# Optimization experiments

Measured on AMD Instinct MI355X. Metric: run time of the kernel, lower is better.

## Reference

```python
import jax, jax.numpy as jnp
import numpy as np
import math

B, S, D, H = 2, 2048, 1024, 16
DH = D // H
FF = 4096
EPS = 1e-5


def _xavier(k, shape):
    lim = math.sqrt(6.0 / (shape[0] + shape[1]))
    return jax.random.uniform(k, shape, jnp.float32, -lim, lim)


def setup_inputs() -> dict:
    key = jax.random.key(0)
    ks = jax.random.split(key, 8)
    return {
        "x": jax.random.normal(ks[0], (B, S, D), jnp.float32),
        "mask": jnp.ones((B, S), jnp.int32),
        "WQ": _xavier(ks[1], (D, D)), "bQ": jnp.zeros((D,), jnp.float32),
        "WK": _xavier(ks[2], (D, D)), "bK": jnp.zeros((D,), jnp.float32),
        "WV": _xavier(ks[3], (D, D)), "bV": jnp.zeros((D,), jnp.float32),
        "WY": _xavier(ks[4], (D, D)), "bY": jnp.zeros((D,), jnp.float32),
        "ln1_w": jnp.ones((D,), jnp.float32), "ln1_b": jnp.zeros((D,), jnp.float32),
        "ln2_w": jnp.ones((D,), jnp.float32), "ln2_b": jnp.zeros((D,), jnp.float32),
        "W1": _xavier(ks[5], (D, FF)), "b1": jnp.zeros((FF,), jnp.float32),
        "W2": _xavier(ks[6], (FF, D)), "b2": jnp.zeros((D,), jnp.float32),
    }


def _layer_norm(x, w, b):
    # manual LayerNorm: biased variance over last dim
    m = jnp.mean(x, axis=-1, keepdims=True)
    v = jnp.mean(jnp.square(x - m), axis=-1, keepdims=True)
    return (x - m) / jnp.sqrt(v + EPS) * w + b


def _attention(x, mask, WQ, bQ, WK, bK, WV, bV, WY, bY):
    b, s, _ = x.shape
    def split(t):  # (B,S,D) -> (B,H,S,DH)
        return t.reshape(b, s, H, DH).transpose(0, 2, 1, 3)
    q = split(x @ WQ + bQ)
    k = split(x @ WK + bK)
    v = split(x @ WV + bV)
    scores = jnp.einsum('bhqd,bhkd->bhqk', q, k) / math.sqrt(DH)
    scores = jnp.where(mask[:, None, None, :] == 0, -jnp.inf, scores)
    w = jax.nn.softmax(scores, axis=-1)
    y = jnp.einsum('bhqk,bhkd->bhqd', w, v)
    y = y.transpose(0, 2, 1, 3).reshape(b, s, D)  # merge heads
    return y @ WY + bY


def reference(x, mask, WQ, bQ, WK, bK, WV, bV, WY, bY,
              ln1_w, ln1_b, ln2_w, ln2_b, W1, b1, W2, b2):
    a = _attention(x, mask, WQ, bQ, WK, bK, WV, bV, WY, bY)
    h = _layer_norm(a + x, ln1_w, ln1_b)
    ff = jax.nn.gelu(h @ W1 + b1, approximate=False) @ W2 + b2
    return _layer_norm(ff + h, ln2_w, ln2_b)
```

## Files before the change

### kernel.cpp

```cpp
#include <hip/hip_runtime.h>
#include <cstdint>
#include <cstddef>

#define B_ 2
#define S_ 2048
#define D_ 1024
#define H_ 16
#define DH_ 64
#define FF_ 4096
#define M_ (B_*S_)
#define MB_ ((size_t)1 << 20)
#define NT_ (S_/64)

using u16 = unsigned short;
using short8 = __attribute__((ext_vector_type(8))) short;
using short4v = __attribute__((ext_vector_type(4))) short;
using floatx4 = __attribute__((ext_vector_type(4))) float;

__device__ __forceinline__ float bf2f(u16 u) {
    return __uint_as_float(((uint32_t)u) << 16);
}
__device__ __forceinline__ u16 f2bf(float f) {
    uint32_t u = __float_as_uint(f);
    u += 0x7fffu + ((u >> 16) & 1u);
    return (u16)(u >> 16);
}
__device__ __forceinline__ uint32_t cvtpk_bf16(float lo, float hi) {
    uint32_t r;
    asm("v_cvt_pk_bf16_f32 %0, %1, %2" : "=v"(r) : "v"(lo), "v"(hi));
    return r;
}
__device__ __forceinline__ void async_copy16(const u16* g, u16* l) {
    __builtin_amdgcn_global_load_lds(
        (const __attribute__((address_space(1))) uint32_t*)g,
        (__attribute__((address_space(3))) uint32_t*)l, 16, 0, 0);
}

__device__ __forceinline__ void gemm_step(
    const u16* Acur, const u16* Bcur, u16* Astg, u16* Bstg, bool pref,
    const u16*& gA, const u16*& gB, int K,
    int w, int wm, int wn, int lm, int quad, floatx4 (&acc)[4][4])
{
    if (pref) {
        async_copy16(gA, Astg + w * 512);
        async_copy16(gA + (size_t)64 * K, Astg + w * 512 + 2048);
        async_copy16(gB, Bstg + w * 512);
        async_copy16(gB + (size_t)64 * K, Bstg + w * 512 + 2048);
        gA += 32; gB += 32;
    }
    short8 af[4], bfr[4];
#pragma unroll
    for (int t4 = 0; t4 < 4; ++t4)
        af[t4] = *(const short8*)&Acur[(wm * 64 + t4 * 16 + lm) * 32 + quad * 8];
#pragma unroll
    for (int t4 = 0; t4 < 4; ++t4)
        bfr[t4] = *(const short8*)&Bcur[(wn * 64 + t4 * 16 + lm) * 32 + quad * 8];
#pragma unroll
    for (int i = 0; i < 4; ++i)
#pragma unroll
        for (int j = 0; j < 4; ++j)
            acc[i][j] = __builtin_amdgcn_mfma_f32_16x16x32_bf16(
                af[i], bfr[j], acc[i][j], 0, 0, 0);
    __syncthreads();
}

__global__ __launch_bounds__(256) void cvt_f32_bf16(
    const float* __restrict__ in, u16* __restrict__ out, int n)
{
    const int i = (blockIdx.x * 256 + threadIdx.x) * 4;
    if (i < n) {
        const float4 v = *(const float4*)(in + i);
        out[i + 0] = f2bf(v.x);
        out[i + 1] = f2bf(v.y);
        out[i + 2] = f2bf(v.z);
        out[i + 3] = f2bf(v.w);
    }
}

__global__ __launch_bounds__(256) void mask_bias(
    const int* __restrict__ mask, float* __restrict__ bias, int n)
{
    const int i = blockIdx.x * 256 + threadIdx.x;
    if (i < n) bias[i] = mask[i] ? 0.f : -1e30f;
}

__global__ void transpose_cvt(const float* __restrict__ in, u16* __restrict__ out,
                              int R, int C) {
    __shared__ float t[32][33];
    const int bx = blockIdx.x * 32, by = blockIdx.y * 32;
    const int tx = threadIdx.x, ty = threadIdx.y;
#pragma unroll
    for (int i = 0; i < 32; i += 8)
        t[ty + i][tx] = in[(size_t)(by + ty + i) * C + bx + tx];
    __syncthreads();
#pragma unroll
    for (int i = 0; i < 32; i += 8)
        out[(size_t)(bx + ty + i) * R + by + tx] = f2bf(t[tx][ty + i]);
}

__global__ void transpose_cvt4(
    const float* __restrict__ WQ, const float* __restrict__ WK,
    const float* __restrict__ WV, const float* __restrict__ WY,
    u16* __restrict__ Wqkvt, u16* __restrict__ WYt)
{
    __shared__ float t[32][33];
    const int zz = blockIdx.z;
    const float* in = zz == 0 ? WQ : zz == 1 ? WK : zz == 2 ? WV : WY;
    u16* out = zz < 3 ? Wqkvt + (size_t)zz * D_ * D_ : WYt;
    const int bx = blockIdx.x * 32, by = blockIdx.y * 32;
    const int tx = threadIdx.x, ty = threadIdx.y;
#pragma unroll
    for (int i = 0; i < 32; i += 8)
        t[ty + i][tx] = in[(size_t)(by + ty + i) * D_ + bx + tx];
    __syncthreads();
#pragma unroll
    for (int i = 0; i < 32; i += 8)
        out[(size_t)(bx + ty + i) * D_ + by + tx] = f2bf(t[tx][ty + i]);
}

template<bool GELU, bool OUT_F32>
__global__ __launch_bounds__(256) void gemm_bt(
    const u16* __restrict__ A, const u16* __restrict__ Bt,
    const float* __restrict__ bias, void* __restrict__ Cout,
    int M, int N, int K)
{
    __shared__ alignas(16) u16 As[2][128 * 32];
    __shared__ alignas(16) u16 Bs[2][128 * 32];
    const int tid = threadIdx.x;
    const int w = tid >> 6, lane = tid & 63;
    const int lm = lane & 15, quad = lane >> 4;
    const int wm = w >> 1, wn = w & 1;

    const int nwg = gridDim.x * gridDim.y;
    int bid = blockIdx.y * gridDim.x + blockIdx.x;
    if ((nwg & 7) == 0) {
        const int cpx = nwg >> 3;
        bid = (bid & 7) * cpx + (bid >> 3);
    }
    const int bx = bid % gridDim.x, by = bid / gridDim.x;
    const size_t m0 = (size_t)by * 128, n0 = (size_t)bx * 128;

    const int rowS = w * 16 + (lane >> 2);
    const int colS = (lane & 3) * 8;
    const u16* gA = A + (m0 + rowS) * K + colS;
    const u16* gB = Bt + (n0 + rowS) * K + colS;

    floatx4 acc[4][4];
    const floatx4 z = {0.f, 0.f, 0.f, 0.f};
#pragma unroll
    for (int i = 0; i < 4; ++i)
#pragma unroll
        for (int j = 0; j < 4; ++j) acc[i][j] = z;

    async_copy16(gA, &As[0][w * 512]);
    async_copy16(gA + (size_t)64 * K, &As[0][w * 512 + 2048]);
    async_copy16(gB, &Bs[0][w * 512]);
    async_copy16(gB + (size_t)64 * K, &Bs[0][w * 512 + 2048]);
    gA += 32; gB += 32;
    __syncthreads();

    const int nk = K >> 5;
    for (int t = 0; t < nk; t += 2) {
        gemm_step(As[0], Bs[0], As[1], Bs[1], true,
                  gA, gB, K, w, wm, wn, lm, quad, acc);
        gemm_step(As[1], Bs[1], As[0], Bs[0], t + 2 < nk,
                  gA, gB, K, w, wm, wn, lm, quad, acc);
    }

#pragma unroll
    for (int i = 0; i < 4; ++i) {
        const size_t r0 = m0 + wm * 64 + i * 16 + quad * 4;
#pragma unroll
        for (int j = 0; j < 4; ++j) {
            const size_t c = n0 + wn * 64 + j * 16 + lm;
            const float bv = bias[c];
#pragma unroll
            for (int t = 0; t < 4; ++t) {
                float v = acc[i][j][t] + bv;
                if (GELU) v = 0.5f * v * (1.f + erff(v * 0.70710678118f));
                if (OUT_F32) ((float*)Cout)[(r0 + t) * (size_t)N + c] = v;
                else         ((u16*)Cout)[(r0 + t) * (size_t)N + c] = f2bf(v);
            }
        }
    }
}

__global__ __launch_bounds__(256) void gemm_bt_skp(
    const u16* __restrict__ A, const u16* __restrict__ Bt,
    const float* __restrict__ bias, float* __restrict__ out0,
    float* __restrict__ Pext, int M, int N, int K)
{
    __shared__ alignas(16) u16 As[2][128 * 32];
    __shared__ alignas(16) u16 Bs[2][128 * 32];
    const int tid = threadIdx.x;
    const int w = tid >> 6, lane = tid & 63;
    const int lm = lane & 15, quad = lane >> 4;
    const int wm = w >> 1, wn = w & 1;
    const int kh = blockIdx.z;
    const int Ks = K / gridDim.z;

    const int nwg = gridDim.x * gridDim.y;
    int bid = blockIdx.y * gridDim.x + blockIdx.x;
    if ((nwg & 7) == 0) {
        const int cpx = nwg >> 3;
        bid = (bid & 7) * cpx + (bid >> 3);
    }
    const int bx = bid % gridDim.x, by = bid / gridDim.x;
    const size_t m0 = (size_t)by * 128, n0 = (size_t)bx * 128;

    const int rowS = w * 16 + (lane >> 2);
    const int colS = (lane & 3) * 8;
    const u16* gA = A + (m0 + rowS) * K + (size_t)kh * Ks + colS;
    const u16* gB = Bt + (n0 + rowS) * K + (size_t)kh * Ks + colS;

    floatx4 acc[4][4];
    const floatx4 z = {0.f, 0.f, 0.f, 0.f};
#pragma unroll
    for (int i = 0; i < 4; ++i)
#pragma unroll
        for (int j = 0; j < 4; ++j) acc[i][j] = z;

    async_copy16(gA, &As[0][w * 512]);
    async_copy16(gA + (size_t)64 * K, &As[0][w * 512 + 2048]);
    async_copy16(gB, &Bs[0][w * 512]);
    async_copy16(gB + (size_t)64 * K, &Bs[0][w * 512 + 2048]);
    gA += 32; gB += 32;
    __syncthreads();

    const int nk = Ks >> 5;
    for (int t = 0; t < nk; t += 2) {
        gemm_step(As[0], Bs[0], As[1], Bs[1], true,
                  gA, gB, K, w, wm, wn, lm, quad, acc);
        gemm_step(As[1], Bs[1], As[0], Bs[0], t + 2 < nk,
                  gA, gB, K, w, wm, wn, lm, quad, acc);
    }

    float* Cout = (kh == 0) ? out0 : Pext + (size_t)(kh - 1) * ((size_t)M * N);
#pragma unroll
    for (int i = 0; i < 4; ++i) {
        const size_t r0 = m0 + wm * 64 + i * 16 + quad * 4;
#pragma unroll
        for (int j = 0; j < 4; ++j) {
            const size_t c = n0 + wn * 64 + j * 16 + lm;
            const float bv = (kh == 0) ? bias[c] : 0.f;
#pragma unroll
            for (int t = 0; t < 4; ++t)
                Cout[(r0 + t) * (size_t)N + c] = acc[i][j][t] + bv;
        }
    }
}

__global__ __launch_bounds__(256) void gemm_bt_sk2(
    const u16* __restrict__ A, const u16* __restrict__ Bt,
    const float* __restrict__ bias, float* __restrict__ Cout,
    int M, int N, int K)
{
    __shared__ alignas(16) u16 As[2][128 * 32];
    __shared__ alignas(16) u16 Bs[2][128 * 32];
    const int tid = threadIdx.x;
    const int w = tid >> 6, lane = tid & 63;
    const int lm = lane & 15, quad = lane >> 4;
    const int wm = w >> 1, wn = w & 1;
    const int kh = blockIdx.z;
    const int Ks = K >> 1;
    const size_t m0 = (size_t)blockIdx.y * 128, n0 = (size_t)blockIdx.x * 128;

    const int rowS = w * 16 + (lane >> 2);
    const int colS = (lane & 3) * 8;
    const u16* gA = A + (m0 + rowS) * K + (size_t)kh * Ks + colS;
    const u16* gB = Bt + (n0 + rowS) * K + (size_t)kh * Ks + colS;

    floatx4 acc[4][4];
    const floatx4 z = {0.f, 0.f, 0.f, 0.f};
#pragma unroll
    for (int i = 0; i < 4; ++i)
#pragma unroll
        for (int j = 0; j < 4; ++j) acc[i][j] = z;

    async_copy16(gA, &As[0][w * 512]);
    async_copy16(gA + (size_t)64 * K, &As[0][w * 512 + 2048]);
    async_copy16(gB, &Bs[0][w * 512]);
    async_copy16(gB + (size_t)64 * K, &Bs[0][w * 512 + 2048]);
    gA += 32; gB += 32;
    __syncthreads();

    const int nk = Ks >> 5;
    for (int t = 0; t < nk; t += 2) {
        gemm_step(As[0], Bs[0], As[1], Bs[1], true,
                  gA, gB, K, w, wm, wn, lm, quad, acc);
        gemm_step(As[1], Bs[1], As[0], Bs[0], t + 2 < nk,
                  gA, gB, K, w, wm, wn, lm, quad, acc);
    }

#pragma unroll
    for (int i = 0; i < 4; ++i) {
        const size_t r0 = m0 + wm * 64 + i * 16 + quad * 4;
#pragma unroll
        for (int j = 0; j < 4; ++j) {
            const size_t c = n0 + wn * 64 + j * 16 + lm;
            const float bv = (kh == 0) ? bias[c] : 0.f;
#pragma unroll
            for (int t = 0; t < 4; ++t)
                atomicAdd(&Cout[(r0 + t) * (size_t)N + c], acc[i][j][t] + bv);
        }
    }
}

__global__ __launch_bounds__(256) void gemm_qkv(
    const u16* __restrict__ A, const u16* __restrict__ Bt,
    const float* __restrict__ bQ, const float* __restrict__ bK,
    const float* __restrict__ bV,
    u16* __restrict__ Qb, u16* __restrict__ Kb, u16* __restrict__ Vt)
{
    const int K = D_, N = 3 * D_;
    __shared__ alignas(16) u16 As[2][128 * 32];
    __shared__ alignas(16) u16 Bs[2][128 * 32];
    const int tid = threadIdx.x;
    const int w = tid >> 6, lane = tid & 63;
    const int lm = lane & 15, quad = lane >> 4;
    const int wm = w >> 1, wn = w & 1;

    const int nwg = gridDim.x * gridDim.y;
    int bid = blockIdx.y * gridDim.x + blockIdx.x;
    if ((nwg & 7) == 0) {
        const int cpx = nwg >> 3;
        bid = (bid & 7) * cpx + (bid >> 3);
    }
    const int bx = bid % gridDim.x, by = bid / gridDim.x;
    const size_t m0 = (size_t)by * 128, n0 = (size_t)bx * 128;

    const int rowS = w * 16 + (lane >> 2);
    const int colS = (lane & 3) * 8;
    const u16* gA = A + (m0 + rowS) * K + colS;
    const u16* gB = Bt + (n0 + rowS) * K + colS;

    floatx4 acc[4][4];
    const floatx4 z = {0.f, 0.f, 0.f, 0.f};
#pragma unroll
    for (int i = 0; i < 4; ++i)
#pragma unroll
        for (int j = 0; j < 4; ++j) acc[i][j] = z;

    async_copy16(gA, &As[0][w * 512]);
    async_copy16(gA + (size_t)64 * K, &As[0][w * 512 + 2048]);
    async_copy16(gB, &Bs[0][w * 512]);
    async_copy16(gB + (size_t)64 * K, &Bs[0][w * 512 + 2048]);
    gA += 32; gB += 32;
    __syncthreads();

    const int nk = K >> 5;
    for (int t = 0; t < nk; t += 2) {
        gemm_step(As[0], Bs[0], As[1], Bs[1], true,
                  gA, gB, K, w, wm, wn, lm, quad, acc);
        gemm_step(As[1], Bs[1], As[0], Bs[0], t + 2 < nk,
                  gA, gB, K, w, wm, wn, lm, quad, acc);
    }

#pragma unroll
    for (int i = 0; i < 4; ++i) {
        const size_t r0 = m0 + wm * 64 + i * 16 + quad * 4;
#pragma unroll
        for (int j = 0; j < 4; ++j) {
            const size_t c = n0 + wn * 64 + j * 16 + lm;
            const int sel = (int)(c >> 10);
            const int col = (int)(c & 1023);
            const float bv = sel == 0 ? bQ[col] : (sel == 1 ? bK[col] : bV[col]);
#pragma unroll
            for (int t = 0; t < 4; ++t) {
                const size_t r = r0 + t;
                const u16 v = f2bf(acc[i][j][t] + bv);
                if (sel == 0)      Qb[r * (size_t)D_ + col] = v;
                else if (sel == 1) Kb[r * (size_t)D_ + col] = v;
                else {
                    const int h = col >> 6, dh = col & 63;
                    const int bb = (int)(r >> 11), s = (int)(r & 2047);
                    Vt[((size_t)((bb * 16 + h) * 64 + dh)) * S_ + s] = v;
                }
            }
        }
    }
}

__global__ __launch_bounds__(256) void attn_kernel(
    const u16* __restrict__ Q, const u16* __restrict__ Kg,
    const u16* __restrict__ Vt, const float* __restrict__ mbias,
    u16* __restrict__ O)
{
    __shared__ alignas(16) u16 Kt[2][64 * 72];
    __shared__ alignas(16) u16 Vs[2][64 * 72];
    const int tid = threadIdx.x, w = tid >> 6, lane = tid & 63;
    const int lm = lane & 15, quad = lane >> 4;
    const int b = blockIdx.y >> 4, h = blockIdx.y & 15;
    const int q0 = blockIdx.x * 64;

    const u16* qp = Q + ((size_t)(b * S_ + q0 + w * 16 + lm)) * D_ + h * 64;
    const short8 bq0 = *(const short8*)(qp + quad * 8);
    const short8 bq1 = *(const short8*)(qp + 32 + quad * 8);

    const int sRow = tid >> 2, sCol = (tid & 3) * 16;
    const u16* gK = Kg + ((size_t)(b * S_ + sRow)) * D_ + h * 64 + sCol;
    const u16* gV = Vt + ((size_t)((b * 16 + h) * 64 + sRow)) * S_ + sCol;

    float mrow = -1e30f, lrow = 0.f;
    floatx4 o[4];
    const floatx4 z = {0.f, 0.f, 0.f, 0.f};
#pragma unroll
    for (int i = 0; i < 4; ++i) o[i] = z;

    const float* bp = mbias + b * S_;
    const float SCL = 0.18033688011112042f;

    short8 rk0 = *(const short8*)(gK);
    short8 rk1 = *(const short8*)(gK + 8);
    short8 rv0 = *(const short8*)(gV);
    short8 rv1 = *(const short8*)(gV + 8);

    for (int it = 0; it < NT_; ++it) {
        u16* kb = Kt[it & 1];
        u16* vb = Vs[it & 1];
        *(short8*)&kb[sRow * 72 + sCol]     = rk0;
        *(short8*)&kb[sRow * 72 + sCol + 8] = rk1;
        *(short8*)&vb[sRow * 72 + sCol]     = rv0;
        *(short8*)&vb[sRow * 72 + sCol + 8] = rv1;
        __syncthreads();
        if (it + 1 < NT_) {
            gK += (size_t)64 * D_; gV += 64;
            rk0 = *(const short8*)(gK);
            rk1 = *(const short8*)(gK + 8);
            rv0 = *(const short8*)(gV);
            rv1 = *(const short8*)(gV + 8);
        }

        floatx4 st[4];
        __builtin_amdgcn_s_setprio(1);
#pragma unroll
        for (int ks = 0; ks < 4; ++ks) {
            floatx4 s = z;
            const short8 ak0 = *(const short8*)&kb[(ks * 16 + lm) * 72 + quad * 8];
            const short8 ak1 = *(const short8*)&kb[(ks * 16 + lm) * 72 + 32 + quad * 8];
            s = __builtin_amdgcn_mfma_f32_16x16x32_bf16(ak0, bq0, s, 0, 0, 0);
            s = __builtin_amdgcn_mfma_f32_16x16x32_bf16(ak1, bq1, s, 0, 0, 0);
            const float4 mb4 = *(const float4*)&bp[it * 64 + ks * 16 + quad * 4];
            st[ks][0] = fmaf(s[0], SCL, mb4.x);
            st[ks][1] = fmaf(s[1], SCL, mb4.y);
            st[ks][2] = fmaf(s[2], SCL, mb4.z);
            st[ks][3] = fmaf(s[3], SCL, mb4.w);
        }
        __builtin_amdgcn_s_setprio(0);

        float t0 = fmaxf(fmaxf(st[0][0], st[0][1]), st[0][2]);
        float t1 = fmaxf(fmaxf(st[0][3], st[1][0]), st[1][1]);
        float t2 = fmaxf(fmaxf(st[1][2], st[1][3]), st[2][0]);
        float t3 = fmaxf(fmaxf(st[2][1], st[2][2]), st[2][3]);
        float t4 = fmaxf(fmaxf(st[3][0], st[3][1]), st[3][2]);
        float tm = fmaxf(fmaxf(t0, t1), t2);
        tm = fmaxf(fmaxf(tm, t3), t4);
        tm = fmaxf(tm, st[3][3]);
        tm = fmaxf(tm, __shfl_xor(tm, 16));
        tm = fmaxf(tm, __shfl_xor(tm, 32));

        if (!__all(tm <= mrow + 8.f)) {
            const float mn = fmaxf(mrow, tm);
            const float al = __builtin_amdgcn_exp2f(mrow - mn);
            mrow = mn;
            lrow *= al;
#pragma unroll
            for (int d = 0; d < 4; ++d) o[d] *= al;
        }

        float rs = 0.f;
#pragma unroll
        for (int ks = 0; ks < 4; ++ks)
#pragma unroll
            for (int r = 0; r < 4; ++r) {
                const float p = __builtin_amdgcn_exp2f(st[ks][r] - mrow);
                st[ks][r] = p; rs += p;
            }
        rs += __shfl_xor(rs, 16);
        rs += __shfl_xor(rs, 32);
        lrow += rs;

        short4v pb[4];
#pragma unroll
        for (int ks = 0; ks < 4; ++ks) {
            uint2 uu;
            uu.x = cvtpk_bf16(st[ks][0], st[ks][1]);
            uu.y = cvtpk_bf16(st[ks][2], st[ks][3]);
            pb[ks] = __builtin_bit_cast(short4v, uu);
        }
        __builtin_amdgcn_s_setprio(1);
#pragma unroll
        for (int d = 0; d < 4; ++d)
#pragma unroll
            for (int ks = 0; ks < 4; ++ks) {
                const short4v av = *(const short4v*)&vb[(d * 16 + lm) * 72 + ks * 16 + quad * 4];
                o[d] = __builtin_amdgcn_mfma_f32_16x16x16bf16_1k(av, pb[ks], o[d], 0, 0, 0);
            }
        __builtin_amdgcn_s_setprio(0);
    }
    const float inv = __builtin_amdgcn_rcpf(lrow);
    u16* op = O + ((size_t)(b * S_ + q0 + w * 16 + lm)) * D_ + h * 64 + quad * 4;
#pragma unroll
    for (int d = 0; d < 4; ++d) {
        uint2 uu;
        uu.x = cvtpk_bf16(o[d][0] * inv, o[d][1] * inv);
        uu.y = cvtpk_bf16(o[d][2] * inv, o[d][3] * inv);
        *(uint2*)(op + d * 16) = uu;
    }
}

template<bool MAIN_F32, bool RESID_F32, bool OUT_F32>
__global__ __launch_bounds__(256) void add_ln(
    const void* __restrict__ mainp, const void* __restrict__ resid,
    const float* __restrict__ gamma, const float* __restrict__ beta,
    void* __restrict__ out)
{
    const int row = blockIdx.x;
    const size_t base = (size_t)row * D_;
    const int t = threadIdx.x;
    const int w = t >> 6, lane = t & 63;
    float v[4];
#pragma unroll
    for (int i = 0; i < 4; ++i) {
        const int c = i * 256 + t;
        const float mv = MAIN_F32 ? ((const float*)mainp)[base + c]
                                  : bf2f(((const u16*)mainp)[base + c]);
        const float rv = RESID_F32 ? ((const float*)resid)[base + c]
                                   : bf2f(((const u16*)resid)[base + c]);
        v[i] = mv + rv;
    }
    float s = v[0] + v[1] + v[2] + v[3];
#pragma unroll
    for (int off = 32; off >= 1; off >>= 1) s += __shfl_xor(s, off);
    __shared__ float red[8];
    if (lane == 0) red[w] = s;
    __syncthreads();
    const float mean = (red[0] + red[1] + red[2] + red[3]) * (1.0f / D_);
    float q = 0.f;
#pragma unroll
    for (int i = 0; i < 4; ++i) { const float dd = v[i] - mean; q += dd * dd; }
#pragma unroll
    for (int off = 32; off >= 1; off >>= 1) q += __shfl_xor(q, off);
    if (lane == 0) red[4 + w] = q;
    __syncthreads();
    const float var = (red[4] + red[5] + red[6] + red[7]) * (1.0f / D_);
    const float rstd = rsqrtf(var + 1e-5f);
#pragma unroll
    for (int i = 0; i < 4; ++i) {
        const int c = i * 256 + t;
        const float o = (v[i] - mean) * rstd * gamma[c] + beta[c];
        if (OUT_F32) ((float*)out)[base + c] = o;
        else         ((u16*)out)[base + c] = f2bf(o);
    }
}

template<int NEXT, bool RESID_F32, bool OUT_F32>
__global__ __launch_bounds__(256) void add_ln_red(
    const float* __restrict__ mainp, const float* __restrict__ Pext,
    const void* __restrict__ resid,
    const float* __restrict__ gamma, const float* __restrict__ beta,
    void* __restrict__ out)
{
    const int row = blockIdx.x;
    const size_t base = (size_t)row * D_;
    const int t = threadIdx.x;
    const int w = t >> 6, lane = t & 63;
    float v[4];
#pragma unroll
    for (int i = 0; i < 4; ++i) {
        const int c = i * 256 + t;
        float s = mainp[base + c];
#pragma unroll
        for (int p = 0; p < NEXT; ++p)
            s += Pext[(size_t)p * ((size_t)M_ * D_) + base + c];
        s += RESID_F32 ? ((const float*)resid)[base + c]
                       : bf2f(((const u16*)resid)[base + c]);
        v[i] = s;
    }
    float s = v[0] + v[1] + v[2] + v[3];
#pragma unroll
    for (int off = 32; off >= 1; off >>= 1) s += __shfl_xor(s, off);
    __shared__ float red[8];
    if (lane == 0) red[w] = s;
    __syncthreads();
    const float mean = (red[0] + red[1] + red[2] + red[3]) * (1.0f / D_);
    float q = 0.f;
#pragma unroll
    for (int i = 0; i < 4; ++i) { const float dd = v[i] - mean; q += dd * dd; }
#pragma unroll
    for (int off = 32; off >= 1; off >>= 1) q += __shfl_xor(q, off);
    if (lane == 0) red[4 + w] = q;
    __syncthreads();
    const float var = (red[4] + red[5] + red[6] + red[7]) * (1.0f / D_);
    const float rstd = rsqrtf(var + 1e-5f);
#pragma unroll
    for (int i = 0; i < 4; ++i) {
        const int c = i * 256 + t;
        const float o = (v[i] - mean) * rstd * gamma[c] + beta[c];
        if (OUT_F32) ((float*)out)[base + c] = o;
        else         ((u16*)out)[base + c] = f2bf(o);
    }
}

extern "C" void kernel_launch(void* const* d_in, const int* in_sizes, int n_in,
                              void* d_out, int out_size, void* d_ws, size_t ws_size,
                              hipStream_t stream)
{
    const float* x   = (const float*)d_in[0];
    const int* mask  = (const int*)d_in[1];
    const float* WQ = (const float*)d_in[2];  const float* bQ = (const float*)d_in[3];
    const float* WK = (const float*)d_in[4];  const float* bK = (const float*)d_in[5];
    const float* WV = (const float*)d_in[6];  const float* bV = (const float*)d_in[7];
    const float* WY = (const float*)d_in[8];  const float* bY = (const float*)d_in[9];
    const float* ln1w = (const float*)d_in[10]; const float* ln1b = (const float*)d_in[11];
    const float* ln2w = (const float*)d_in[12]; const float* ln2b = (const float*)d_in[13];
    const float* W1 = (const float*)d_in[14]; const float* b1 = (const float*)d_in[15];
    const float* W2 = (const float*)d_in[16]; const float* b2 = (const float*)d_in[17];

    char* ws = (char*)d_ws;
    u16* xb    = (u16*)(ws + 0  * MB_);
    u16* Wqkvt = (u16*)(ws + 8  * MB_);
    u16* WYt   = (u16*)(ws + 14 * MB_);
    u16* Qb    = (u16*)(ws + 16 * MB_);
    u16* Kb    = (u16*)(ws + 24 * MB_);
    u16* Vt    = (u16*)(ws + 32 * MB_);
    u16* Yat   = (u16*)(ws + 40 * MB_);
    float* Ypf = (float*)(ws + 16 * MB_);
    u16* hbf   = (u16*)(ws + 8  * MB_);
    u16* W1t   = (u16*)(ws + 0  * MB_);
    u16* G     = (u16*)(ws + 16 * MB_);
    u16* W2t   = (u16*)(ws + 0  * MB_);
    float* mb  = (float*)(ws + 48 * MB_);
    float* Pext = (float*)(ws + 49 * MB_);

    const size_t PART = (size_t)M_ * D_ * sizeof(float);
    const bool ws1 = ws_size >= 49 * MB_ + 1 * PART;
    const bool ws3 = ws_size >= 49 * MB_ + 3 * PART;

    const dim3 tb(32, 8);

    cvt_f32_bf16<<<(M_*D_)/1024, 256, 0, stream>>>(x, xb, M_*D_);
    mask_bias<<<(B_*S_)/256, 256, 0, stream>>>(mask, mb, B_*S_);
    transpose_cvt4<<<dim3(D_/32, D_/32, 4), tb, 0, stream>>>(WQ, WK, WV, WY, Wqkvt, WYt);

    gemm_qkv<<<dim3(3*D_/128, M_/128), 256, 0, stream>>>(xb, Wqkvt, bQ, bK, bV, Qb, Kb, Vt);

    attn_kernel<<<dim3(S_/64, B_*H_), 256, 0, stream>>>(Qb, Kb, Vt, mb, Yat);

    if (ws1) {
        gemm_bt_skp<<<dim3(D_/128, M_/128, 2), 256, 0, stream>>>(
            Yat, WYt, bY, Ypf, Pext, M_, D_, D_);
        add_ln_red<1,true,false><<<M_, 256, 0, stream>>>(Ypf, Pext, x, ln1w, ln1b, hbf);
    } else {
        hipMemsetAsync(Ypf, 0, PART, stream);
        gemm_bt_sk2<<<dim3(D_/128, M_/128, 2), 256, 0, stream>>>(
            Yat, WYt, bY, Ypf, M_, D_, D_);
        add_ln<true,true,false><<<M_, 256, 0, stream>>>(Ypf, x, ln1w, ln1b, hbf);
    }

    transpose_cvt<<<dim3(FF_/32, D_/32), tb, 0, stream>>>(W1, W1t, D_, FF_);
    gemm_bt<true,false><<<dim3(FF_/128, M_/128), 256, 0, stream>>>(hbf, W1t, b1, G, M_, FF_, D_);

    transpose_cvt<<<dim3(D_/32, FF_/32), tb, 0, stream>>>(W2, W2t, FF_, D_);

    if (ws3) {
        gemm_bt_skp<<<dim3(D_/128, M_/128, 4), 256, 0, stream>>>(
            G, W2t, b2, (float*)d_out, Pext, M_, D_, FF_);
        add_ln_red<3,false,true><<<M_, 256, 0, stream>>>(
            (float*)d_out, Pext, hbf, ln2w, ln2b, d_out);
    } else if (ws1) {
        gemm_bt_skp<<<dim3(D_/128, M_/128, 2), 256, 0, stream>>>(
            G, W2t, b2, (float*)d_out, Pext, M_, D_, FF_);
        add_ln_red<1,false,true><<<M_, 256, 0, stream>>>(
            (float*)d_out, Pext, hbf, ln2w, ln2b, d_out);
    } else {
        hipMemsetAsync(d_out, 0, (size_t)M_ * D_ * 4, stream);
        gemm_bt_sk2<<<dim3(D_/128, M_/128, 2), 256, 0, stream>>>(
            G, W2t, b2, (float*)d_out, M_, D_, FF_);
        add_ln<true,false,true><<<M_, 256, 0, stream>>>(
            (float*)d_out, hbf, ln2w, ln2b, d_out);
    }
}
```

Measured before the change: 447.5 us.

## Triple-buffer GEMM LDS pipeline, add fast GELU, tree reductions, drop 4-way split-K

All GEMM kernels switch from a double-buffered LDS loop with a full __syncthreads per step to a three-stage ring that keeps two K-tiles of global->LDS copies in flight. Each step waits only for the oldest copy (vmcnt) before a bare s_barrier. Exact erff in the FF1 GELU epilogue is replaced by an Abramowitz-Stegun polynomial using rcp/exp2. The attention softmax max and sum become balanced trees. The 4-way split-K path for the W2 GEMM is removed, so it always uses 2-way split when workspace allows. The ring uses 50% more LDS per block, which may lower occupancy, and the GELU approximation adds small error.

```diff
diff --git a/kernel.cpp b/kernel.cpp
--- a/kernel.cpp
+++ b/kernel.cpp
@@ -36,32 +36,66 @@
         (__attribute__((address_space(3))) uint32_t*)l, 16, 0, 0);
 }
 
-__device__ __forceinline__ void gemm_step(
-    const u16* Acur, const u16* Bcur, u16* Astg, u16* Bstg, bool pref,
-    const u16*& gA, const u16*& gB, int K,
+__device__ __forceinline__ float gelu_f(float v) {
+    const float ax = fabsf(v) * 0.70710678118f;
+    const float t  = __builtin_amdgcn_rcpf(fmaf(0.3275911f, ax, 1.f));
+    float p = fmaf(1.061405429f, t, -1.453152027f);
+    p = fmaf(p, t, 1.421413741f);
+    p = fmaf(p, t, -0.284496736f);
+    p = fmaf(p, t, 0.254829592f);
+    p *= t;
+    const float e = __builtin_amdgcn_exp2f(ax * ax * -1.4426950408889634f);
+    float erfv = fmaf(-p, e, 1.f);
+    erfv = copysignf(erfv, v);
+    return 0.5f * v * (1.f + erfv);
+}
+
+__device__ __forceinline__ void stage4(const u16* gA, const u16* gB,
+                                       u16* lA, u16* lB, int w, int K) {
+    async_copy16(gA, lA + w * 512);
+    async_copy16(gA + (size_t)64 * K, lA + w * 512 + 2048);
+    async_copy16(gB, lB + w * 512);
+    async_copy16(gB + (size_t)64 * K, lB + w * 512 + 2048);
+}
+
+__device__ __forceinline__ void gemm_core(
+    const u16* gA, const u16* gB, int K, int nk,
+    u16 (&As)[3][128 * 32], u16 (&Bs)[3][128 * 32],
     int w, int wm, int wn, int lm, int quad, floatx4 (&acc)[4][4])
 {
-    if (pref) {
-        async_copy16(gA, Astg + w * 512);
-        async_copy16(gA + (size_t)64 * K, Astg + w * 512 + 2048);
-        async_copy16(gB, Bstg + w * 512);
-        async_copy16(gB + (size_t)64 * K, Bstg + w * 512 + 2048);
-        gA += 32; gB += 32;
-    }
-    short8 af[4], bfr[4];
-#pragma unroll
-    for (int t4 = 0; t4 < 4; ++t4)
-        af[t4] = *(const short8*)&Acur[(wm * 64 + t4 * 16 + lm) * 32 + quad * 8];
-#pragma unroll
-    for (int t4 = 0; t4 < 4; ++t4)
-        bfr[t4] = *(const short8*)&Bcur[(wn * 64 + t4 * 16 + lm) * 32 + quad * 8];
-#pragma unroll
-    for (int i = 0; i < 4; ++i)
-#pragma unroll
-        for (int j = 0; j < 4; ++j)
-            acc[i][j] = __builtin_amdgcn_mfma_f32_16x16x32_bf16(
-                af[i], bfr[j], acc[i][j], 0, 0, 0);
-    __syncthreads();
+    stage4(gA, gB, As[0], Bs[0], w, K); gA += 32; gB += 32;
+    stage4(gA, gB, As[1], Bs[1], w, K); gA += 32; gB += 32;
+    asm volatile("s_waitcnt vmcnt(4)" ::: "memory");
+    __builtin_amdgcn_s_barrier();
+
+    int cur = 0, stg = 2;
+    for (int t = 0; t < nk; ++t) {
+        if (t + 2 < nk) {
+            stage4(gA, gB, As[stg], Bs[stg], w, K);
+            gA += 32; gB += 32;
+        }
+        const u16* Ac = As[cur];
+        const u16* Bc = Bs[cur];
+        short8 af[4], bfr[4];
+#pragma unroll
+        for (int t4 = 0; t4 < 4; ++t4)
+            af[t4] = *(const short8*)&Ac[(wm * 64 + t4 * 16 + lm) * 32 + quad * 8];
+#pragma unroll
+        for (int t4 = 0; t4 < 4; ++t4)
+            bfr[t4] = *(const short8*)&Bc[(wn * 64 + t4 * 16 + lm) * 32 + quad * 8];
+#pragma unroll
+        for (int i = 0; i < 4; ++i)
+#pragma unroll
+            for (int j = 0; j < 4; ++j)
+                acc[i][j] = __builtin_amdgcn_mfma_f32_16x16x32_bf16(
+                    af[i], bfr[j], acc[i][j], 0, 0, 0);
+
+        if (t + 2 < nk)      asm volatile("s_waitcnt vmcnt(4)" ::: "memory");
+        else if (t + 1 < nk) asm volatile("s_waitcnt vmcnt(0)" ::: "memory");
+        if (t + 1 < nk) __builtin_amdgcn_s_barrier();
+        cur = (cur == 2) ? 0 : cur + 1;
+        stg = (stg == 2) ? 0 : stg + 1;
+    }
 }
 
 __global__ __launch_bounds__(256) void cvt_f32_bf16(
@@ -124,8 +158,8 @@
     const float* __restrict__ bias, void* __restrict__ Cout,
     int M, int N, int K)
 {
-    __shared__ alignas(16) u16 As[2][128 * 32];
-    __shared__ alignas(16) u16 Bs[2][128 * 32];
+    __shared__ alignas(16) u16 As[3][128 * 32];
+    __shared__ alignas(16) u16 Bs[3][128 * 32];
     const int tid = threadIdx.x;
     const int w = tid >> 6, lane = tid & 63;
     const int lm = lane & 15, quad = lane >> 4;
@@ -152,20 +186,7 @@
 #pragma unroll
         for (int j = 0; j < 4; ++j) acc[i][j] = z;
 
-    async_copy16(gA, &As[0][w * 512]);
-    async_copy16(gA + (size_t)64 * K, &As[0][w * 512 + 2048]);
-    async_copy16(gB, &Bs[0][w * 512]);
-    async_copy16(gB + (size_t)64 * K, &Bs[0][w * 512 + 2048]);
-    gA += 32; gB += 32;
-    __syncthreads();
-
-    const int nk = K >> 5;
-    for (int t = 0; t < nk; t += 2) {
-        gemm_step(As[0], Bs[0], As[1], Bs[1], true,
-                  gA, gB, K, w, wm, wn, lm, quad, acc);
-        gemm_step(As[1], Bs[1], As[0], Bs[0], t + 2 < nk,
-                  gA, gB, K, w, wm, wn, lm, quad, acc);
-    }
+    gemm_core(gA, gB, K, K >> 5, As, Bs, w, wm, wn, lm, quad, acc);
 
 #pragma unroll
     for (int i = 0; i < 4; ++i) {
@@ -177,7 +198,7 @@
 #pragma unroll
             for (int t = 0; t < 4; ++t) {
                 float v = acc[i][j][t] + bv;
-                if (GELU) v = 0.5f * v * (1.f + erff(v * 0.70710678118f));
+                if (GELU) v = gelu_f(v);
                 if (OUT_F32) ((float*)Cout)[(r0 + t) * (size_t)N + c] = v;
                 else         ((u16*)Cout)[(r0 + t) * (size_t)N + c] = f2bf(v);
             }
@@ -190,8 +211,8 @@
     const float* __restrict__ bias, float* __restrict__ out0,
     float* __restrict__ Pext, int M, int N, int K)
 {
-    __shared__ alignas(16) u16 As[2][128 * 32];
-    __shared__ alignas(16) u16 Bs[2][128 * 32];
+    __shared__ alignas(16) u16 As[3][128 * 32];
+    __shared__ alignas(16) u16 Bs[3][128 * 32];
     const int tid = threadIdx.x;
     const int w = tid >> 6, lane = tid & 63;
     const int lm = lane & 15, quad = lane >> 4;
@@ -220,20 +241,7 @@
 #pragma unroll
         for (int j = 0; j < 4; ++j) acc[i][j] = z;
 
-    async_copy16(gA, &As[0][w * 512]);
-    async_copy16(gA + (size_t)64 * K, &As[0][w * 512 + 2048]);
-    async_copy16(gB, &Bs[0][w * 512]);
-    async_copy16(gB + (size_t)64 * K, &Bs[0][w * 512 + 2048]);
-    gA += 32; gB += 32;
-    __syncthreads();
-
-    const int nk = Ks >> 5;
-    for (int t = 0; t < nk; t += 2) {
-        gemm_step(As[0], Bs[0], As[1], Bs[1], true,
-                  gA, gB, K, w, wm, wn, lm, quad, acc);
-        gemm_step(As[1], Bs[1], As[0], Bs[0], t + 2 < nk,
-                  gA, gB, K, w, wm, wn, lm, quad, acc);
-    }
+    gemm_core(gA, gB, K, Ks >> 5, As, Bs, w, wm, wn, lm, quad, acc);
 
     float* Cout = (kh == 0) ? out0 : Pext + (size_t)(kh - 1) * ((size_t)M * N);
 #pragma unroll
@@ -255,8 +263,8 @@
     const float* __restrict__ bias, float* __restrict__ Cout,
     int M, int N, int K)
 {
-    __shared__ alignas(16) u16 As[2][128 * 32];
-    __shared__ alignas(16) u16 Bs[2][128 * 32];
+    __shared__ alignas(16) u16 As[3][128 * 32];
+    __shared__ alignas(16) u16 Bs[3][128 * 32];
     const int tid = threadIdx.x;
     const int w = tid >> 6, lane = tid & 63;
     const int lm = lane & 15, quad = lane >> 4;
@@ -277,20 +285,7 @@
 #pragma unroll
         for (int j = 0; j < 4; ++j) acc[i][j] = z;
 
-    async_copy16(gA, &As[0][w * 512]);
-    async_copy16(gA + (size_t)64 * K, &As[0][w * 512 + 2048]);
-    async_copy16(gB, &Bs[0][w * 512]);
-    async_copy16(gB + (size_t)64 * K, &Bs[0][w * 512 + 2048]);
-    gA += 32; gB += 32;
-    __syncthreads();
-
-    const int nk = Ks >> 5;
-    for (int t = 0; t < nk; t += 2) {
-        gemm_step(As[0], Bs[0], As[1], Bs[1], true,
-                  gA, gB, K, w, wm, wn, lm, quad, acc);
-        gemm_step(As[1], Bs[1], As[0], Bs[0], t + 2 < nk,
-                  gA, gB, K, w, wm, wn, lm, quad, acc);
-    }
+    gemm_core(gA, gB, K, Ks >> 5, As, Bs, w, wm, wn, lm, quad, acc);
 
 #pragma unroll
     for (int i = 0; i < 4; ++i) {
@@ -312,9 +307,9 @@
     const float* __restrict__ bV,
     u16* __restrict__ Qb, u16* __restrict__ Kb, u16* __restrict__ Vt)
 {
-    const int K = D_, N = 3 * D_;
-    __shared__ alignas(16) u16 As[2][128 * 32];
-    __shared__ alignas(16) u16 Bs[2][128 * 32];
+    const int K = D_;
+    __shared__ alignas(16) u16 As[3][128 * 32];
+    __shared__ alignas(16) u16 Bs[3][128 * 32];
     const int tid = threadIdx.x;
     const int w = tid >> 6, lane = tid & 63;
     const int lm = lane & 15, quad = lane >> 4;
@@ -341,20 +336,7 @@
 #pragma unroll
         for (int j = 0; j < 4; ++j) acc[i][j] = z;
 
-    async_copy16(gA, &As[0][w * 512]);
-    async_copy16(gA + (size_t)64 * K, &As[0][w * 512 + 2048]);
-    async_copy16(gB, &Bs[0][w * 512]);
-    async_copy16(gB + (size_t)64 * K, &Bs[0][w * 512 + 2048]);
-    gA += 32; gB += 32;
-    __syncthreads();
-
-    const int nk = K >> 5;
-    for (int t = 0; t < nk; t += 2) {
-        gemm_step(As[0], Bs[0], As[1], Bs[1], true,
-                  gA, gB, K, w, wm, wn, lm, quad, acc);
-        gemm_step(As[1], Bs[1], As[0], Bs[0], t + 2 < nk,
-                  gA, gB, K, w, wm, wn, lm, quad, acc);
-    }
+    gemm_core(gA, gB, K, K >> 5, As, Bs, w, wm, wn, lm, quad, acc);
 
 #pragma unroll
     for (int i = 0; i < 4; ++i) {
@@ -448,14 +430,11 @@
         }
         __builtin_amdgcn_s_setprio(0);
 
-        float t0 = fmaxf(fmaxf(st[0][0], st[0][1]), st[0][2]);
-        float t1 = fmaxf(fmaxf(st[0][3], st[1][0]), st[1][1]);
-        float t2 = fmaxf(fmaxf(st[1][2], st[1][3]), st[2][0]);
-        float t3 = fmaxf(fmaxf(st[2][1], st[2][2]), st[2][3]);
-        float t4 = fmaxf(fmaxf(st[3][0], st[3][1]), st[3][2]);
-        float tm = fmaxf(fmaxf(t0, t1), t2);
-        tm = fmaxf(fmaxf(tm, t3), t4);
-        tm = fmaxf(tm, st[3][3]);
+        float m01 = fmaxf(fmaxf(st[0][0], st[0][1]), fmaxf(st[0][2], st[0][3]));
+        float m11 = fmaxf(fmaxf(st[1][0], st[1][1]), fmaxf(st[1][2], st[1][3]));
+        float m21 = fmaxf(fmaxf(st[2][0], st[2][1]), fmaxf(st[2][2], st[2][3]));
+        float m31 = fmaxf(fmaxf(st[3][0], st[3][1]), fmaxf(st[3][2], st[3][3]));
+        float tm = fmaxf(fmaxf(m01, m11), fmaxf(m21, m31));
         tm = fmaxf(tm, __shfl_xor(tm, 16));
         tm = fmaxf(tm, __shfl_xor(tm, 32));
 
@@ -468,14 +447,15 @@
             for (int d = 0; d < 4; ++d) o[d] *= al;
         }
 
-        float rs = 0.f;
-#pragma unroll
-        for (int ks = 0; ks < 4; ++ks)
-#pragma unroll
-            for (int r = 0; r < 4; ++r) {
-                const float p = __builtin_amdgcn_exp2f(st[ks][r] - mrow);
-                st[ks][r] = p; rs += p;
-            }
+        float sks[4];
+#pragma unroll
+        for (int ks = 0; ks < 4; ++ks) {
+#pragma unroll
+            for (int r = 0; r < 4; ++r)
+                st[ks][r] = __builtin_amdgcn_exp2f(st[ks][r] - mrow);
+            sks[ks] = (st[ks][0] + st[ks][1]) + (st[ks][2] + st[ks][3]);
+        }
+        float rs = (sks[0] + sks[1]) + (sks[2] + sks[3]);
         rs += __shfl_xor(rs, 16);
         rs += __shfl_xor(rs, 32);
         lrow += rs;
@@ -635,7 +615,6 @@
 
     const size_t PART = (size_t)M_ * D_ * sizeof(float);
     const bool ws1 = ws_size >= 49 * MB_ + 1 * PART;
-    const bool ws3 = ws_size >= 49 * MB_ + 3 * PART;
 
     const dim3 tb(32, 8);
 
@@ -663,12 +642,7 @@
 
     transpose_cvt<<<dim3(D_/32, FF_/32), tb, 0, stream>>>(W2, W2t, FF_, D_);
 
-    if (ws3) {
-        gemm_bt_skp<<<dim3(D_/128, M_/128, 4), 256, 0, stream>>>(
-            G, W2t, b2, (float*)d_out, Pext, M_, D_, FF_);
-        add_ln_red<3,false,true><<<M_, 256, 0, stream>>>(
-            (float*)d_out, Pext, hbf, ln2w, ln2b, d_out);
-    } else if (ws1) {
+    if (ws1) {
         gemm_bt_skp<<<dim3(D_/128, M_/128, 2), 256, 0, stream>>>(
             G, W2t, b2, (float*)d_out, Pext, M_, D_, FF_);
         add_ln_red<1,false,true><<<M_, 256, 0, stream>>>(
```

After: 405.4 us. -9.4%, faster.
